# Kernel optimization log

Hardware: AMD Instinct MI355X
Metric: run time of the kernel (lower is better)

## Reference

```python
import jax, jax.numpy as jnp
import numpy as np

H = 16  # n_heads (from init_kwargs)


def l2norm(x, eps=1e-6):
    return x * jax.lax.rsqrt(jnp.sum(x * x, axis=-1, keepdims=True) + eps)


def causal_conv1d(x, w, b):
    # depthwise causal conv: x (B,T,D), w (D,k), b (D,). Matches torch
    # Conv1d(d,d,k,groups=d,padding=k-1) followed by [:, :, :T] truncation.
    T = x.shape[1]
    k = w.shape[1]
    xp = jnp.pad(x, ((0, 0), (k - 1, 0), (0, 0)))
    y = b
    for j in range(k):  # k=4 taps, fixed small loop
        y = y + xp[:, j:j + T, :] * w[:, j]
    return y


def setup_inputs():
    key = jax.random.key(0)
    ks = jax.random.split(key, 16)
    B, T, D, kc = 2, 2048, 1024, 4
    d = D // H
    s = 1.0 / np.sqrt(D)
    return {
        "x": jax.random.normal(ks[0], (B, T, D), jnp.float32),
        "Wq": jax.random.normal(ks[1], (D, D), jnp.float32) * s,
        "Wk": jax.random.normal(ks[2], (D, D), jnp.float32) * s,
        "Wv": jax.random.normal(ks[3], (D, D), jnp.float32) * s,
        "Wo": jax.random.normal(ks[4], (D, D), jnp.float32) * s,
        "Wg": jax.random.normal(ks[5], (D, D), jnp.float32) * s,
        "Wb": jax.random.normal(ks[6], (D, H), jnp.float32) * s,
        "cq_w": jax.random.normal(ks[7], (D, kc), jnp.float32) * 0.3,
        "cq_b": jax.random.normal(ks[8], (D,), jnp.float32) * 0.1,
        "ck_w": jax.random.normal(ks[9], (D, kc), jnp.float32) * 0.3,
        "ck_b": jax.random.normal(ks[10], (D,), jnp.float32) * 0.1,
        "cv_w": jax.random.normal(ks[11], (D, kc), jnp.float32) * 0.3,
        "cv_b": jax.random.normal(ks[12], (D,), jnp.float32) * 0.1,
        "nw": jnp.ones((d,), jnp.float32),
    }


def reference(x, Wq, Wk, Wv, Wo, Wg, Wb, cq_w, cq_b, ck_w, ck_b, cv_w, cv_b, nw):
    B, T, D = x.shape
    d = D // H
    q = l2norm(jax.nn.silu(causal_conv1d(x @ Wq, cq_w, cq_b)).reshape(B, T, H, d))
    q = q / jnp.sqrt(jnp.asarray(d, x.dtype))
    k = l2norm(jax.nn.silu(causal_conv1d(x @ Wk, ck_w, ck_b)).reshape(B, T, H, d))
    v = jax.nn.silu(causal_conv1d(x @ Wv, cv_w, cv_b)).reshape(B, T, H, d)
    gate = (x @ Wg).reshape(B, T, H, d)
    beta = jax.nn.sigmoid(x @ Wb)[..., None]  # (B,T,H,1)

    def step(S, qkvb):
        q_t, k_t, v_t, b_t = qkvb  # (B,H,d), (B,H,d), (B,H,d), (B,H,1)
        err = (v_t - jnp.einsum('bhk,bhkv->bhv', k_t, S)) * b_t
        S = S + jnp.einsum('bhk,bhv->bhkv', k_t, err)
        o_t = jnp.einsum('bhk,bhkv->bhv', q_t, S)
        return S, o_t

    S0 = jnp.zeros((B, H, d, d), x.dtype)
    xs = (q.transpose(1, 0, 2, 3), k.transpose(1, 0, 2, 3),
          v.transpose(1, 0, 2, 3), beta.transpose(1, 0, 2, 3))
    _, oT = jax.lax.scan(step, S0, xs)
    o = oT.transpose(1, 0, 2, 3)  # (B,T,H,d)
    # RMSNorm over head_dim
    o = o * jax.lax.rsqrt(jnp.mean(o * o, axis=-1, keepdims=True) + 1e-5) * nw
    o = o * jax.nn.silu(gate)
    return o.reshape(B, T, D) @ Wo
```

## Files before the change

kernel.cpp:

```cpp
#include <hip/hip_runtime.h>
#include <hip/hip_bf16.h>

typedef __attribute__((ext_vector_type(8))) short short8;
typedef __attribute__((ext_vector_type(4))) float f32x4;

#define TSEQ 2048
#define DMODEL 1024
#define NH 16
#define HD 64
#define PLANE 4194304

__device__ __forceinline__ ushort f2bf(float f) {
    union { float f; unsigned int u; } c; c.f = f;
    unsigned int u = c.u + 0x7fffu + ((c.u >> 16) & 1u);
    return (ushort)(u >> 16);
}

__device__ __forceinline__ float bf2f(ushort u) {
    union { unsigned int i; float f; } c; c.i = ((unsigned int)u) << 16;
    return c.f;
}

__device__ __forceinline__ void split2(float x, ushort& h, ushort& l) {
    h = f2bf(x);
    float r = x - bf2f(h);
    l = f2bf(r);
}

__device__ __forceinline__ float silu_f(float y) {
    return y / (1.f + __expf(-y));
}

__device__ __forceinline__ void gl_lds16(const float* g, float* l) {
    __builtin_amdgcn_global_load_lds(
        (__attribute__((address_space(1))) void*)g,
        (__attribute__((address_space(3))) void*)l, 16, 0, 0);
}

__global__ void gdn_cvt_x(const float* __restrict__ x, ushort* __restrict__ xb) {
    int i = blockIdx.x * 256 + threadIdx.x;
    float4 v = ((const float4*)x)[i];
    ushort4 o;
    o.x = f2bf(v.x); o.y = f2bf(v.y); o.z = f2bf(v.z); o.w = f2bf(v.w);
    ((ushort4*)xb)[i] = o;
}

__global__ void gdn_cvt_w(const float* __restrict__ Wq, const float* __restrict__ Wk,
                          const float* __restrict__ Wv, const float* __restrict__ Wg,
                          const float* __restrict__ Wo, ushort* __restrict__ wt) {
    __shared__ float tile[32][33];
    int z = blockIdx.z;
    const float* W = (z == 0) ? Wq : (z == 1) ? Wk : (z == 2) ? Wv : (z == 3) ? Wg : Wo;
    int n0 = blockIdx.x * 32, k0 = blockIdx.y * 32;
    int tx = threadIdx.x, ty = threadIdx.y;
    #pragma unroll
    for (int j = 0; j < 32; j += 8)
        tile[ty + j][tx] = W[(size_t)(k0 + ty + j) * DMODEL + n0 + tx];
    __syncthreads();
    ushort* o = wt + (size_t)z * DMODEL * DMODEL;
    #pragma unroll
    for (int j = 0; j < 32; j += 8)
        o[(size_t)(n0 + ty + j) * DMODEL + k0 + tx] = f2bf(tile[tx][ty + j]);
}

__global__ void gdn_beta(const float* __restrict__ x, const float* __restrict__ Wb,
                         float* __restrict__ betaT) {
    __shared__ float xs[16][DMODEL];
    int tid = threadIdx.x;
    int m0 = blockIdx.x * 16;
    #pragma unroll
    for (int i = 0; i < 16; i++) {
        int idx = i * 256 + tid;
        int row = idx >> 8, c4 = idx & 255;
        *(float4*)&xs[row][c4 * 4] =
            *(const float4*)&x[(size_t)(m0 + row) * DMODEL + c4 * 4];
    }
    __syncthreads();
    int h = tid & 15, mi = tid >> 4;
    float acc = 0.f;
    for (int k = 0; k < DMODEL; ++k)
        acc += xs[mi][k] * Wb[k * NH + h];
    int m = m0 + mi;
    int b = m >> 11, t = m & (TSEQ - 1);
    betaT[((b * NH + h) << 11) + t] = 1.f / (1.f + __expf(-acc));
}

#define LDT 40
__global__ __launch_bounds__(256) void gdn_gemm(const ushort* __restrict__ A,
                                                const ushort* __restrict__ Bt,
                                                float* __restrict__ outF,
                                                size_t planeStride) {
    __shared__ ushort As[128 * LDT];
    __shared__ ushort Bs[128 * LDT];
    int tid = threadIdx.x;
    int lane = tid & 63, wid = tid >> 6;
    int wm = wid & 1, wn = wid >> 1;
    int l15 = lane & 15, quad = lane >> 4;
    int bm = blockIdx.x, bn = blockIdx.y;
    const int K = DMODEL;

    f32x4 acc[4][4];
    #pragma unroll
    for (int i = 0; i < 4; i++)
        #pragma unroll
        for (int j = 0; j < 4; j++)
            acc[i][j] = (f32x4){0.f, 0.f, 0.f, 0.f};

    for (int kt = 0; kt < K; kt += 32) {
        __syncthreads();
        #pragma unroll
        for (int i = 0; i < 2; i++) {
            int ch = tid * 2 + i;
            int row = ch >> 2, q = ch & 3;
            uint4 av = ((const uint4*)A)[((bm * 128 + row) * K + kt) / 8 + q];
            *(uint4*)&As[row * LDT + q * 8] = av;
            uint4 bv = ((const uint4*)Bt)[((bn * 128 + row) * K + kt) / 8 + q];
            *(uint4*)&Bs[row * LDT + q * 8] = bv;
        }
        __syncthreads();
        short8 af[4], bf[4];
        #pragma unroll
        for (int i = 0; i < 4; i++) {
            af[i] = *(const short8*)&As[(wm * 64 + i * 16 + l15) * LDT + quad * 8];
            bf[i] = *(const short8*)&Bs[(wn * 64 + i * 16 + l15) * LDT + quad * 8];
        }
        #pragma unroll
        for (int mt = 0; mt < 4; mt++)
            #pragma unroll
            for (int nt = 0; nt < 4; nt++)
                acc[mt][nt] = __builtin_amdgcn_mfma_f32_16x16x32_bf16(
                    af[mt], bf[nt], acc[mt][nt], 0, 0, 0);
    }

    #pragma unroll
    for (int mt = 0; mt < 4; mt++)
        #pragma unroll
        for (int nt = 0; nt < 4; nt++)
            #pragma unroll
            for (int r = 0; r < 4; r++) {
                int row = bm * 128 + wm * 64 + mt * 16 + quad * 4 + r;
                int col = bn * 128 + wn * 64 + nt * 16 + l15;
                outF[(size_t)(col >> 10) * planeStride + (size_t)row * 1024 + (col & 1023)]
                    = acc[mt][nt][r];
            }
}

__global__ void gdn_conv(const float* __restrict__ pre,
                         const float* __restrict__ cqw, const float* __restrict__ cqb,
                         const float* __restrict__ ckw, const float* __restrict__ ckb,
                         const float* __restrict__ cvw, const float* __restrict__ cvb,
                         float* __restrict__ qn, float* __restrict__ kn, float* __restrict__ vn) {
    int m = blockIdx.x;
    int which = blockIdx.y;
    int t = m & (TSEQ - 1);
    const float* cw = (which == 0) ? cqw : (which == 1) ? ckw : cvw;
    const float* cb = (which == 0) ? cqb : (which == 1) ? ckb : cvb;
    float* dst = (which == 0) ? qn : (which == 1) ? kn : vn;
    int c = threadIdx.x * 4;

    float w[4][4];
    #pragma unroll
    for (int i = 0; i < 4; i++) {
        float4 t4 = ((const float4*)cw)[c + i];
        w[i][0] = t4.x; w[i][1] = t4.y; w[i][2] = t4.z; w[i][3] = t4.w;
    }
    float4 bias = ((const float4*)cb)[threadIdx.x];
    float y[4] = {bias.x, bias.y, bias.z, bias.w};

    const float* src = pre + (size_t)which * PLANE + (size_t)m * DMODEL + c;
    #pragma unroll
    for (int j = 0; j < 4; j++) {
        int tt = t - 3 + j;
        if (tt >= 0) {
            float4 xv = *(const float4*)(src + (long)(j - 3) * DMODEL);
            y[0] += xv.x * w[0][j];
            y[1] += xv.y * w[1][j];
            y[2] += xv.z * w[2][j];
            y[3] += xv.w * w[3][j];
        }
    }
    #pragma unroll
    for (int i = 0; i < 4; i++) y[i] = silu_f(y[i]);

    if (which < 2) {
        float ss = y[0]*y[0] + y[1]*y[1] + y[2]*y[2] + y[3]*y[3];
        ss += __shfl_xor(ss, 1);
        ss += __shfl_xor(ss, 2);
        ss += __shfl_xor(ss, 4);
        ss += __shfl_xor(ss, 8);
        float sc = rsqrtf(ss + 1e-6f);
        if (which == 0) sc *= 0.125f;
        #pragma unroll
        for (int i = 0; i < 4; i++) y[i] *= sc;
    }
    float4 o; o.x = y[0]; o.y = y[1]; o.z = y[2]; o.w = y[3];
    ((float4*)(dst + (size_t)m * 1024))[threadIdx.x] = o;
}

__global__ __launch_bounds__(256) void gdn_chunk(
    const float* __restrict__ kn, const float* __restrict__ vn,
    const float* __restrict__ betaT,
    ushort* __restrict__ WTst, ushort* __restrict__ U0st,
    float* __restrict__ Pst, float* __restrict__ Rst)
{
    __shared__ ushort Khi[64 * 72], Klo[64 * 72];
    __shared__ ushort KThi[64 * 72], KTlo[64 * 72];
    __shared__ ushort XThi[128 * 72], XTlo[128 * 72];
    __shared__ ushort Mneghi[64 * 72], Mneglo[64 * 72];
    __shared__ float  Xf[64 * 132];
    __shared__ float  MmDiag[4 * 16 * 20];
    __shared__ float  bet[64];

    int c = blockIdx.x, bh = blockIdx.y;
    int b = bh >> 4, h = bh & 15;
    int tid = threadIdx.x;
    int w = tid >> 6, lane = tid & 63;
    int l15 = lane & 15, quad = lane >> 4;
    size_t gbase = ((size_t)(b * TSEQ + c * 64)) * DMODEL + h * 64;
    size_t u = (size_t)bh * 32 + c;

    if (tid < 64) bet[tid] = betaT[((size_t)bh << 11) + c * 64 + tid];
    #pragma unroll
    for (int i = 0; i < 18; i++) {
        ((uint*)XThi)[tid + 256 * i] = 0u;
        ((uint*)XTlo)[tid + 256 * i] = 0u;
    }
    __syncthreads();

    #pragma unroll
    for (int i = 0; i < 4; i++) {
        int idx = tid + 256 * i;
        int r = idx >> 4, c4 = (idx & 15) * 4;
        float4 kv = *(const float4*)&kn[gbase + (size_t)r * DMODEL + c4];
        float4 vv = *(const float4*)&vn[gbase + (size_t)r * DMODEL + c4];
        float br = bet[r];
        float4 xk; xk.x = br * kv.x; xk.y = br * kv.y; xk.z = br * kv.z; xk.w = br * kv.w;
        float4 xv; xv.x = br * vv.x; xv.y = br * vv.y; xv.z = br * vv.z; xv.w = br * vv.w;
        *(float4*)&Xf[r * 132 + c4] = xk;
        *(float4*)&Xf[r * 132 + 64 + c4] = xv;
        ushort h0, l0, h1, l1, h2, l2, h3, l3;
        split2(kv.x, h0, l0); split2(kv.y, h1, l1);
        split2(kv.z, h2, l2); split2(kv.w, h3, l3);
        ((uint*)&Khi[r * 72 + c4])[0] = (uint)h0 | ((uint)h1 << 16);
        ((uint*)&Khi[r * 72 + c4])[1] = (uint)h2 | ((uint)h3 << 16);
        ((uint*)&Klo[r * 72 + c4])[0] = (uint)l0 | ((uint)l1 << 16);
        ((uint*)&Klo[r * 72 + c4])[1] = (uint)l2 | ((uint)l3 << 16);
        KThi[(c4 + 0) * 72 + r] = h0; KThi[(c4 + 1) * 72 + r] = h1;
        KThi[(c4 + 2) * 72 + r] = h2; KThi[(c4 + 3) * 72 + r] = h3;
        KTlo[(c4 + 0) * 72 + r] = l0; KTlo[(c4 + 1) * 72 + r] = l1;
        KTlo[(c4 + 2) * 72 + r] = l2; KTlo[(c4 + 3) * 72 + r] = l3;
    }
    __syncthreads();

    {
        f32x4 mAcc[4];
        #pragma unroll
        for (int tn = 0; tn < 4; tn++) mAcc[tn] = (f32x4){0.f, 0.f, 0.f, 0.f};
        #pragma unroll
        for (int ks = 0; ks < 2; ks++) {
            short8 aH = *(const short8*)&Khi[(16 * w + l15) * 72 + ks * 32 + quad * 8];
            short8 aL = *(const short8*)&Klo[(16 * w + l15) * 72 + ks * 32 + quad * 8];
            #pragma unroll
            for (int tn = 0; tn < 4; tn++) {
                short8 bH = *(const short8*)&Khi[(16 * tn + l15) * 72 + ks * 32 + quad * 8];
                short8 bL = *(const short8*)&Klo[(16 * tn + l15) * 72 + ks * 32 + quad * 8];
                mAcc[tn] = __builtin_amdgcn_mfma_f32_16x16x32_bf16(aH, bH, mAcc[tn], 0, 0, 0);
                mAcc[tn] = __builtin_amdgcn_mfma_f32_16x16x32_bf16(aH, bL, mAcc[tn], 0, 0, 0);
                mAcc[tn] = __builtin_amdgcn_mfma_f32_16x16x32_bf16(aL, bH, mAcc[tn], 0, 0, 0);
            }
        }
        #pragma unroll
        for (int tn = 0; tn < 4; tn++) {
            #pragma unroll
            for (int r = 0; r < 4; r++) {
                int row = 16 * w + quad * 4 + r;
                int col = tn * 16 + l15;
                float val = mAcc[tn][r] * bet[row];
                ushort hh = 0, ll = 0;
                if (col < row) {
                    float nv = -val;
                    hh = f2bf(nv);
                    ll = f2bf(nv - bf2f(hh));
                }
                Mneghi[row * 72 + col] = hh;
                Mneglo[row * 72 + col] = ll;
                if (tn == w) MmDiag[w * 320 + (row & 15) * 20 + l15] = val;
            }
        }
    }
    __syncthreads();

    #pragma unroll 1
    for (int st = 0; st < 4; st++) {
        int tb = st * 16;
        if (st) {
            f32x4 acc2[2];
            #pragma unroll
            for (int e = 0; e < 2; e++) {
                int tn = 2 * w + e;
                #pragma unroll
                for (int r = 0; r < 4; r++)
                    acc2[e][r] = Xf[(tb + quad * 4 + r) * 132 + tn * 16 + l15];
            }
            #pragma unroll
            for (int ks = 0; ks < 2; ks++) {
                short8 aH = *(const short8*)&Mneghi[(tb + l15) * 72 + ks * 32 + quad * 8];
                short8 aL = *(const short8*)&Mneglo[(tb + l15) * 72 + ks * 32 + quad * 8];
                #pragma unroll
                for (int e = 0; e < 2; e++) {
                    int tn = 2 * w + e;
                    short8 bH = *(const short8*)&XThi[(tn * 16 + l15) * 72 + ks * 32 + quad * 8];
                    short8 bL = *(const short8*)&XTlo[(tn * 16 + l15) * 72 + ks * 32 + quad * 8];
                    acc2[e] = __builtin_amdgcn_mfma_f32_16x16x32_bf16(aH, bH, acc2[e], 0, 0, 0);
                    acc2[e] = __builtin_amdgcn_mfma_f32_16x16x32_bf16(aH, bL, acc2[e], 0, 0, 0);
                    acc2[e] = __builtin_amdgcn_mfma_f32_16x16x32_bf16(aL, bH, acc2[e], 0, 0, 0);
                }
            }
            #pragma unroll
            for (int e = 0; e < 2; e++) {
                int tn = 2 * w + e;
                #pragma unroll
                for (int r = 0; r < 4; r++)
                    Xf[(tb + quad * 4 + r) * 132 + tn * 16 + l15] = acc2[e][r];
            }
        }
        __syncthreads();

        if (tid < 128) {
            const int j = tid;
            const float* MD = &MmDiag[st * 320];
            float xr[16];
            #pragma unroll
            for (int sb = 0; sb < 4; sb++) {
                float b4[4];
                #pragma unroll
                for (int i = 0; i < 4; i++)
                    b4[i] = Xf[(tb + sb * 4 + i) * 132 + j];
                #pragma unroll
                for (int u4 = 0; u4 < sb; u4++) {
                    #pragma unroll
                    for (int i = 0; i < 4; i++) {
                        float4 m4 = *(const float4*)&MD[(sb * 4 + i) * 20 + u4 * 4];
                        b4[i] -= m4.x * xr[u4 * 4 + 0] + m4.y * xr[u4 * 4 + 1]
                               + m4.z * xr[u4 * 4 + 2] + m4.w * xr[u4 * 4 + 3];
                    }
                }
                float x0 = b4[0];
                float x1 = b4[1] - MD[(sb * 4 + 1) * 20 + sb * 4 + 0] * x0;
                float x2 = b4[2] - MD[(sb * 4 + 2) * 20 + sb * 4 + 0] * x0
                                 - MD[(sb * 4 + 2) * 20 + sb * 4 + 1] * x1;
                float x3 = b4[3] - MD[(sb * 4 + 3) * 20 + sb * 4 + 0] * x0
                                 - MD[(sb * 4 + 3) * 20 + sb * 4 + 1] * x1
                                 - MD[(sb * 4 + 3) * 20 + sb * 4 + 2] * x2;
                xr[sb * 4 + 0] = x0; xr[sb * 4 + 1] = x1;
                xr[sb * 4 + 2] = x2; xr[sb * 4 + 3] = x3;
            }
            ushort hs[16], ls[16];
            #pragma unroll
            for (int i = 0; i < 16; i++) split2(xr[i], hs[i], ls[i]);
            uint4 ph0, ph1, pl0, pl1;
            ph0.x = (uint)hs[0] | ((uint)hs[1] << 16);  ph0.y = (uint)hs[2] | ((uint)hs[3] << 16);
            ph0.z = (uint)hs[4] | ((uint)hs[5] << 16);  ph0.w = (uint)hs[6] | ((uint)hs[7] << 16);
            ph1.x = (uint)hs[8] | ((uint)hs[9] << 16);  ph1.y = (uint)hs[10] | ((uint)hs[11] << 16);
            ph1.z = (uint)hs[12] | ((uint)hs[13] << 16); ph1.w = (uint)hs[14] | ((uint)hs[15] << 16);
            pl0.x = (uint)ls[0] | ((uint)ls[1] << 16);  pl0.y = (uint)ls[2] | ((uint)ls[3] << 16);
            pl0.z = (uint)ls[4] | ((uint)ls[5] << 16);  pl0.w = (uint)ls[6] | ((uint)ls[7] << 16);
            pl1.x = (uint)ls[8] | ((uint)ls[9] << 16);  pl1.y = (uint)ls[10] | ((uint)ls[11] << 16);
            pl1.z = (uint)ls[12] | ((uint)ls[13] << 16); pl1.w = (uint)ls[14] | ((uint)ls[15] << 16);
            *(uint4*)&XThi[j * 72 + tb] = ph0;  *(uint4*)&XThi[j * 72 + tb + 8] = ph1;
            *(uint4*)&XTlo[j * 72 + tb] = pl0;  *(uint4*)&XTlo[j * 72 + tb + 8] = pl1;
            if (j < 64) {
                ushort* wdst = WTst + u * 4096 + j * 64 + tb;
                *(uint4*)wdst = ph0; *(uint4*)(wdst + 8) = ph1;
            } else {
                ushort* udst = U0st + u * 4096 + (size_t)tb * 64 + (j - 64);
                #pragma unroll
                for (int i = 0; i < 16; i++) udst[i * 64] = hs[i];
            }
        }
        __syncthreads();
    }

    {
        f32x4 pAcc[4], rAcc[4];
        #pragma unroll
        for (int tn = 0; tn < 4; tn++) {
            pAcc[tn] = (f32x4){0.f, 0.f, 0.f, 0.f};
            rAcc[tn] = (f32x4){0.f, 0.f, 0.f, 0.f};
        }
        #pragma unroll
        for (int ks = 0; ks < 2; ks++) {
            short8 aH = *(const short8*)&XThi[(16 * w + l15) * 72 + ks * 32 + quad * 8];
            short8 aL = *(const short8*)&XTlo[(16 * w + l15) * 72 + ks * 32 + quad * 8];
            short8 cH = *(const short8*)&KThi[(16 * w + l15) * 72 + ks * 32 + quad * 8];
            short8 cL = *(const short8*)&KTlo[(16 * w + l15) * 72 + ks * 32 + quad * 8];
            #pragma unroll
            for (int tn = 0; tn < 4; tn++) {
                short8 bH = *(const short8*)&KThi[(16 * tn + l15) * 72 + ks * 32 + quad * 8];
                short8 bL = *(const short8*)&KTlo[(16 * tn + l15) * 72 + ks * 32 + quad * 8];
                pAcc[tn] = __builtin_amdgcn_mfma_f32_16x16x32_bf16(aH, bH, pAcc[tn], 0, 0, 0);
                pAcc[tn] = __builtin_amdgcn_mfma_f32_16x16x32_bf16(aH, bL, pAcc[tn], 0, 0, 0);
                pAcc[tn] = __builtin_amdgcn_mfma_f32_16x16x32_bf16(aL, bH, pAcc[tn], 0, 0, 0);
                short8 uH = *(const short8*)&XThi[(64 + 16 * tn + l15) * 72 + ks * 32 + quad * 8];
                short8 uL = *(const short8*)&XTlo[(64 + 16 * tn + l15) * 72 + ks * 32 + quad * 8];
                rAcc[tn] = __builtin_amdgcn_mfma_f32_16x16x32_bf16(cH, uH, rAcc[tn], 0, 0, 0);
                rAcc[tn] = __builtin_amdgcn_mfma_f32_16x16x32_bf16(cH, uL, rAcc[tn], 0, 0, 0);
                rAcc[tn] = __builtin_amdgcn_mfma_f32_16x16x32_bf16(cL, uH, rAcc[tn], 0, 0, 0);
            }
        }
        float* Po = Pst + u * 4096;
        float* Ro = Rst + u * 4096;
        #pragma unroll
        for (int tn = 0; tn < 4; tn++) {
            #pragma unroll
            for (int r = 0; r < 4; r++) {
                int row = 16 * w + quad * 4 + r;
                int col = tn * 16 + l15;
                Po[row * 64 + col] = pAcc[tn][r];
                Ro[row * 64 + col] = rAcc[tn][r];
            }
        }
    }
}

__global__ __launch_bounds__(256) void gdn_sstep(const float* __restrict__ Pst,
                                                 const float* __restrict__ Rst,
                                                 float* __restrict__ S0st)
{
    __shared__ float PTl[2][4096];
    __shared__ float Ssh[64][17];
    int bh = blockIdx.x >> 2, cg = blockIdx.x & 3;
    int tid = threadIdx.x;
    int t0 = (tid & 15) * 4;
    int j = tid >> 4;
    int jg = cg * 16 + j;
    int wv = tid >> 6, ln = tid & 63;

    #pragma unroll
    for (int i = 0; i < 4; i++) Ssh[t0 + i][j] = 0.f;

    {
        size_t ub0 = (size_t)bh * 32 * 4096;
        #pragma unroll
        for (int q = 0; q < 4; q++) {
            int seg = q * 4 + wv;
            gl_lds16(Pst + ub0 + seg * 256 + ln * 4, &PTl[0][seg * 256]);
        }
    }
    __syncthreads();

    for (int c = 0; c < 32; c++) {
        size_t ub = ((size_t)bh * 32 + c) * 4096;
        int cur = c & 1;
        if (c + 1 < 32) {
            size_t ub2 = ub + 4096;
            #pragma unroll
            for (int q = 0; q < 4; q++) {
                int seg = q * 4 + wv;
                gl_lds16(Pst + ub2 + seg * 256 + ln * 4, &PTl[cur ^ 1][seg * 256]);
            }
        }
        float sold[4], acc[4];
        #pragma unroll
        for (int i = 0; i < 4; i++) {
            sold[i] = Ssh[t0 + i][j];
            acc[i] = Rst[ub + (size_t)(t0 + i) * 64 + jg] + sold[i];
        }
        float sub0 = 0.f, sub1 = 0.f, sub2 = 0.f, sub3 = 0.f;
        #pragma unroll 8
        for (int uu = 0; uu < 64; uu++) {
            float4 pt = *(const float4*)&PTl[cur][uu * 64 + t0];
            float sv = Ssh[uu][j];
            sub0 = fmaf(pt.x, sv, sub0);
            sub1 = fmaf(pt.y, sv, sub1);
            sub2 = fmaf(pt.z, sv, sub2);
            sub3 = fmaf(pt.w, sv, sub3);
        }
        __syncthreads();
        Ssh[t0 + 0][j] = acc[0] - sub0;
        Ssh[t0 + 1][j] = acc[1] - sub1;
        Ssh[t0 + 2][j] = acc[2] - sub2;
        Ssh[t0 + 3][j] = acc[3] - sub3;
        #pragma unroll
        for (int i = 0; i < 4; i++)
            S0st[ub + (size_t)(t0 + i) * 64 + jg] = sold[i];
        __syncthreads();
    }
}

__global__ __launch_bounds__(256) void gdn_opass(
    const float* __restrict__ qn, const float* __restrict__ kn,
    const float* __restrict__ S0st, const ushort* __restrict__ WTst,
    const ushort* __restrict__ U0st, float* __restrict__ otmp2)
{
    __shared__ float Qs[64][65];
    __shared__ float KE[64][65];
    __shared__ float S0s[64][65];
    __shared__ float GT[4096];
    __shared__ ushort Wu[4096];
    __shared__ ushort Uu[4096];

    int c = blockIdx.x, bh = blockIdx.y;
    int b = bh >> 4, h = bh & 15;
    int tid = threadIdx.x;
    size_t gbase = ((size_t)(b * TSEQ + c * 64)) * DMODEL + h * 64;
    size_t u = (size_t)bh * 32 + c;

    #pragma unroll
    for (int i = 0; i < 4; i++) {
        int idx = tid + 256 * i;
        int r = idx >> 4, d4 = (idx & 15) * 4;
        float4 qv = *(const float4*)&qn[gbase + (size_t)r * DMODEL + d4];
        float4 kv = *(const float4*)&kn[gbase + (size_t)r * DMODEL + d4];
        float4 sv = *(const float4*)&S0st[u * 4096 + (size_t)idx * 4];
        Qs[r][d4 + 0] = qv.x; Qs[r][d4 + 1] = qv.y; Qs[r][d4 + 2] = qv.z; Qs[r][d4 + 3] = qv.w;
        KE[r][d4 + 0] = kv.x; KE[r][d4 + 1] = kv.y; KE[r][d4 + 2] = kv.z; KE[r][d4 + 3] = kv.w;
        S0s[r][d4 + 0] = sv.x; S0s[r][d4 + 1] = sv.y; S0s[r][d4 + 2] = sv.z; S0s[r][d4 + 3] = sv.w;
    }
    #pragma unroll
    for (int i = 0; i < 2; i++) {
        int idx = tid + 256 * i;
        uint4 w8 = *(const uint4*)&WTst[u * 4096 + (size_t)idx * 8];
        uint4 u8 = *(const uint4*)&U0st[u * 4096 + (size_t)idx * 8];
        *(uint4*)&Wu[idx * 8] = w8;
        *(uint4*)&Uu[idx * 8] = u8;
    }
    __syncthreads();

    int t0 = (tid & 15) * 4, s0 = (tid >> 4) * 4;

    float g[4][4];
    #pragma unroll
    for (int i = 0; i < 4; i++)
        #pragma unroll
        for (int j = 0; j < 4; j++) g[i][j] = 0.f;
    #pragma unroll 8
    for (int kk = 0; kk < 64; kk++) {
        float qt[4], kt[4];
        #pragma unroll
        for (int i = 0; i < 4; i++) qt[i] = Qs[t0 + i][kk];
        #pragma unroll
        for (int j = 0; j < 4; j++) kt[j] = KE[s0 + j][kk];
        #pragma unroll
        for (int i = 0; i < 4; i++)
            #pragma unroll
            for (int j = 0; j < 4; j++) g[i][j] = fmaf(qt[i], kt[j], g[i][j]);
    }
    float e[4][4];
    #pragma unroll
    for (int i = 0; i < 4; i++)
        #pragma unroll
        for (int j = 0; j < 4; j++) e[i][j] = 0.f;
    #pragma unroll 8
    for (int uu = 0; uu < 64; uu++) {
        ushort4 wv = *(const ushort4*)&Wu[uu * 64 + t0];
        float w0 = bf2f(wv.x), w1 = bf2f(wv.y), w2 = bf2f(wv.z), w3 = bf2f(wv.w);
        float s4[4];
        #pragma unroll
        for (int j = 0; j < 4; j++) s4[j] = S0s[uu][s0 + j];
        #pragma unroll
        for (int j = 0; j < 4; j++) {
            e[0][j] = fmaf(w0, s4[j], e[0][j]);
            e[1][j] = fmaf(w1, s4[j], e[1][j]);
            e[2][j] = fmaf(w2, s4[j], e[2][j]);
            e[3][j] = fmaf(w3, s4[j], e[3][j]);
        }
    }
    #pragma unroll
    for (int i = 0; i < 4; i++)
        #pragma unroll
        for (int jj = 0; jj < 4; jj++)
            GT[(s0 + jj) * 64 + t0 + i] = (s0 + jj <= t0 + i) ? g[i][jj] : 0.f;
    __syncthreads();
    #pragma unroll
    for (int i = 0; i < 4; i++) {
        ushort4 uv = *(const ushort4*)&Uu[(t0 + i) * 64 + s0];
        KE[t0 + i][s0 + 0] = bf2f(uv.x) - e[i][0];
        KE[t0 + i][s0 + 1] = bf2f(uv.y) - e[i][1];
        KE[t0 + i][s0 + 2] = bf2f(uv.z) - e[i][2];
        KE[t0 + i][s0 + 3] = bf2f(uv.w) - e[i][3];
    }
    __syncthreads();

    float o[4][4];
    #pragma unroll
    for (int i = 0; i < 4; i++)
        #pragma unroll
        for (int j = 0; j < 4; j++) o[i][j] = 0.f;
    #pragma unroll 8
    for (int kk = 0; kk < 64; kk++) {
        float qt[4], s4[4];
        #pragma unroll
        for (int i = 0; i < 4; i++) qt[i] = Qs[t0 + i][kk];
        #pragma unroll
        for (int j = 0; j < 4; j++) s4[j] = S0s[kk][s0 + j];
        #pragma unroll
        for (int i = 0; i < 4; i++)
            #pragma unroll
            for (int j = 0; j < 4; j++) o[i][j] = fmaf(qt[i], s4[j], o[i][j]);
    }
    #pragma unroll 8
    for (int ss = 0; ss < 64; ss++) {
        float4 gt = *(const float4*)&GT[ss * 64 + t0];
        float e4[4];
        #pragma unroll
        for (int j = 0; j < 4; j++) e4[j] = KE[ss][s0 + j];
        #pragma unroll
        for (int j = 0; j < 4; j++) {
            o[0][j] = fmaf(gt.x, e4[j], o[0][j]);
            o[1][j] = fmaf(gt.y, e4[j], o[1][j]);
            o[2][j] = fmaf(gt.z, e4[j], o[2][j]);
            o[3][j] = fmaf(gt.w, e4[j], o[3][j]);
        }
    }
    size_t obase = ((size_t)bh * 16 + (s0 >> 2)) * TSEQ + c * 64;
    #pragma unroll
    for (int i = 0; i < 4; i++) {
        float4 ov; ov.x = o[i][0]; ov.y = o[i][1]; ov.z = o[i][2]; ov.w = o[i][3];
        ((float4*)otmp2)[obase + t0 + i] = ov;
    }
}

__global__ void gdn_fuse(const float* __restrict__ otmp2, const float* __restrict__ pre,
                         const float* __restrict__ nw, ushort* __restrict__ ofused) {
    int m = blockIdx.x;
    int b = m >> 11, t = m & (TSEQ - 1);
    int tid = threadIdx.x;
    float4 o = ((const float4*)otmp2)[((size_t)((b * NH + (tid >> 4)) * 16 + (tid & 15))) * TSEQ + t];
    float ss = o.x*o.x + o.y*o.y + o.z*o.z + o.w*o.w;
    ss += __shfl_xor(ss, 1);
    ss += __shfl_xor(ss, 2);
    ss += __shfl_xor(ss, 4);
    ss += __shfl_xor(ss, 8);
    float r = rsqrtf(ss * (1.f / 64.f) + 1e-5f);
    float4 nwv = ((const float4*)nw)[tid & 15];
    float4 g = ((const float4*)(pre + 3 * (size_t)PLANE + (size_t)m * DMODEL))[tid];
    ushort4 out;
    out.x = f2bf(o.x * r * nwv.x * silu_f(g.x));
    out.y = f2bf(o.y * r * nwv.y * silu_f(g.y));
    out.z = f2bf(o.z * r * nwv.z * silu_f(g.z));
    out.w = f2bf(o.w * r * nwv.w * silu_f(g.w));
    ((ushort4*)ofused)[m * 256 + tid] = out;
}

extern "C" void kernel_launch(void* const* d_in, const int* in_sizes, int n_in,
                              void* d_out, int out_size, void* d_ws, size_t ws_size,
                              hipStream_t stream) {
    const float* x    = (const float*)d_in[0];
    const float* Wq   = (const float*)d_in[1];
    const float* Wk   = (const float*)d_in[2];
    const float* Wv   = (const float*)d_in[3];
    const float* Wo   = (const float*)d_in[4];
    const float* Wg   = (const float*)d_in[5];
    const float* Wb   = (const float*)d_in[6];
    const float* cq_w = (const float*)d_in[7];
    const float* cq_b = (const float*)d_in[8];
    const float* ck_w = (const float*)d_in[9];
    const float* ck_b = (const float*)d_in[10];
    const float* cv_w = (const float*)d_in[11];
    const float* cv_b = (const float*)d_in[12];
    const float* nw   = (const float*)d_in[13];

    char* ws = (char*)d_ws;
    ushort* xb     = (ushort*)(ws);
    ushort* wt     = (ushort*)(ws + 8388608);
    float*  pre    = (float*)(ws + 18874368);
    float*  qn     = (float*)(ws + 85983232);
    float*  kn     = (float*)(ws + 102760448);
    float*  vn     = (float*)(ws + 119537664);
    float*  betaT  = (float*)(ws + 136314880);
    float*  otmp2  = (float*)(ws + 136577024);
    ushort* ofused = (ushort*)(ws + 153354240);

    float*  Pst  = pre;
    float*  Rst  = pre + PLANE;
    float*  S0st = pre + 2 * PLANE;
    ushort* WTst = xb;
    ushort* U0st = ofused;

    gdn_cvt_x<<<4096, 256, 0, stream>>>(x, xb);
    gdn_cvt_w<<<dim3(32, 32, 5), dim3(32, 8), 0, stream>>>(Wq, Wk, Wv, Wg, Wo, wt);
    gdn_beta<<<256, 256, 0, stream>>>(x, Wb, betaT);
    gdn_gemm<<<dim3(32, 32), 256, 0, stream>>>(xb, wt, pre, (size_t)PLANE);
    gdn_conv<<<dim3(4096, 3), 256, 0, stream>>>(pre, cq_w, cq_b, ck_w, ck_b, cv_w, cv_b,
                                                qn, kn, vn);
    gdn_chunk<<<dim3(32, 32), 256, 0, stream>>>(kn, vn, betaT, WTst, U0st, Pst, Rst);
    gdn_sstep<<<128, 256, 0, stream>>>(Pst, Rst, S0st);
    gdn_opass<<<dim3(32, 32), 256, 0, stream>>>(qn, kn, S0st, WTst, U0st, otmp2);
    gdn_fuse<<<4096, 256, 0, stream>>>(otmp2, pre, nw, ofused);
    gdn_gemm<<<dim3(32, 8), 256, 0, stream>>>(ofused, wt + 4 * 1024 * 1024,
                                              (float*)d_out, (size_t)0);
}
```

Measured before the change: 459.5 us.

## Triple-buffer P/R chunk loads and transpose S in gdn_sstep to use one barrier

The state-propagation kernel now prefetches both P and the R chunk (stored transposed by the producer) two chunks ahead into triple-buffered LDS. It keeps the running state transposed and double-buffered so each step needs a single barrier and reads S as float4. Manual vmcnt waits replace __syncthreads. This targets the serial latency of the 32-chunk recurrence, at the cost of fragile hand-tuned waitcnt counts and more LDS use.

After: 433.6 us. 5.6% less time.

```diff
diff --git a/kernel.cpp b/kernel.cpp
--- a/kernel.cpp
+++ b/kernel.cpp
@@ -417,7 +417,7 @@
                 int row = 16 * w + quad * 4 + r;
                 int col = tn * 16 + l15;
                 Po[row * 64 + col] = pAcc[tn][r];
-                Ro[row * 64 + col] = rAcc[tn][r];
+                Ro[col * 64 + row] = rAcc[tn][r];
             }
         }
     }
@@ -427,64 +427,78 @@
                                                  const float* __restrict__ Rst,
                                                  float* __restrict__ S0st)
 {
-    __shared__ float PTl[2][4096];
-    __shared__ float Ssh[64][17];
+    __shared__ float PTl[3][4096];
+    __shared__ float Rl[3][1024];
+    __shared__ float SshT[2][16][72];
+
     int bh = blockIdx.x >> 2, cg = blockIdx.x & 3;
     int tid = threadIdx.x;
     int t0 = (tid & 15) * 4;
-    int j = tid >> 4;
+    int j  = tid >> 4;
     int jg = cg * 16 + j;
     int wv = tid >> 6, ln = tid & 63;
 
-    #pragma unroll
-    for (int i = 0; i < 4; i++) Ssh[t0 + i][j] = 0.f;
-
-    {
-        size_t ub0 = (size_t)bh * 32 * 4096;
-        #pragma unroll
-        for (int q = 0; q < 4; q++) {
-            int seg = q * 4 + wv;
-            gl_lds16(Pst + ub0 + seg * 256 + ln * 4, &PTl[0][seg * 256]);
-        }
-    }
-    __syncthreads();
-
-    for (int c = 0; c < 32; c++) {
-        size_t ub = ((size_t)bh * 32 + c) * 4096;
-        int cur = c & 1;
-        if (c + 1 < 32) {
-            size_t ub2 = ub + 4096;
-            #pragma unroll
-            for (int q = 0; q < 4; q++) {
-                int seg = q * 4 + wv;
-                gl_lds16(Pst + ub2 + seg * 256 + ln * 4, &PTl[cur ^ 1][seg * 256]);
-            }
-        }
-        float sold[4], acc[4];
-        #pragma unroll
-        for (int i = 0; i < 4; i++) {
-            sold[i] = Ssh[t0 + i][j];
-            acc[i] = Rst[ub + (size_t)(t0 + i) * 64 + jg] + sold[i];
-        }
+    size_t ubase = (size_t)bh * 32 * 4096;
+
+    *(float4*)&SshT[0][j][t0] = (float4){0.f, 0.f, 0.f, 0.f};
+
+    #pragma unroll
+    for (int t = 0; t < 2; t++) {
+        size_t ub = ubase + (size_t)t * 4096;
+        #pragma unroll
+        for (int q = 0; q < 4; q++)
+            gl_lds16(Pst + ub + (wv * 4 + q) * 256 + ln * 4, &PTl[t][(wv * 4 + q) * 256]);
+        gl_lds16(Rst + ub + cg * 1024 + wv * 256 + ln * 4, &Rl[t][wv * 256]);
+    }
+    asm volatile("s_waitcnt vmcnt(5)" ::: "memory");
+    asm volatile("s_waitcnt lgkmcnt(0)" ::: "memory");
+    __builtin_amdgcn_s_barrier();
+
+    int cur3 = 0;
+    #pragma unroll 1
+    for (int c = 0; c < 32; ++c) {
+        int cur = c & 1, nxt = cur ^ 1;
+        if (c + 2 < 32) {
+            int b3 = cur3 + 2; if (b3 >= 3) b3 -= 3;
+            size_t ub2 = ubase + (size_t)(c + 2) * 4096;
+            #pragma unroll
+            for (int q = 0; q < 4; q++)
+                gl_lds16(Pst + ub2 + (wv * 4 + q) * 256 + ln * 4, &PTl[b3][(wv * 4 + q) * 256]);
+            gl_lds16(Rst + ub2 + cg * 1024 + wv * 256 + ln * 4, &Rl[b3][wv * 256]);
+        }
+        float4 sold = *(const float4*)&SshT[cur][j][t0];
+        size_t ub = ubase + (size_t)c * 4096;
+        S0st[ub + (size_t)(t0 + 0) * 64 + jg] = sold.x;
+        S0st[ub + (size_t)(t0 + 1) * 64 + jg] = sold.y;
+        S0st[ub + (size_t)(t0 + 2) * 64 + jg] = sold.z;
+        S0st[ub + (size_t)(t0 + 3) * 64 + jg] = sold.w;
+        float4 racc = *(const float4*)&Rl[cur3][j * 64 + t0];
         float sub0 = 0.f, sub1 = 0.f, sub2 = 0.f, sub3 = 0.f;
-        #pragma unroll 8
-        for (int uu = 0; uu < 64; uu++) {
-            float4 pt = *(const float4*)&PTl[cur][uu * 64 + t0];
-            float sv = Ssh[uu][j];
-            sub0 = fmaf(pt.x, sv, sub0);
-            sub1 = fmaf(pt.y, sv, sub1);
-            sub2 = fmaf(pt.z, sv, sub2);
-            sub3 = fmaf(pt.w, sv, sub3);
-        }
-        __syncthreads();
-        Ssh[t0 + 0][j] = acc[0] - sub0;
-        Ssh[t0 + 1][j] = acc[1] - sub1;
-        Ssh[t0 + 2][j] = acc[2] - sub2;
-        Ssh[t0 + 3][j] = acc[3] - sub3;
-        #pragma unroll
-        for (int i = 0; i < 4; i++)
-            S0st[ub + (size_t)(t0 + i) * 64 + jg] = sold[i];
-        __syncthreads();
+        #pragma unroll
+        for (int u4 = 0; u4 < 16; u4++) {
+            float4 sv = *(const float4*)&SshT[cur][j][u4 * 4];
+            #pragma unroll
+            for (int e = 0; e < 4; e++) {
+                float4 pt = *(const float4*)&PTl[cur3][(u4 * 4 + e) * 64 + t0];
+                float s1 = (e == 0) ? sv.x : (e == 1) ? sv.y : (e == 2) ? sv.z : sv.w;
+                sub0 = fmaf(pt.x, s1, sub0);
+                sub1 = fmaf(pt.y, s1, sub1);
+                sub2 = fmaf(pt.z, s1, sub2);
+                sub3 = fmaf(pt.w, s1, sub3);
+            }
+        }
+        float4 snew;
+        snew.x = sold.x + racc.x - sub0;
+        snew.y = sold.y + racc.y - sub1;
+        snew.z = sold.z + racc.z - sub2;
+        snew.w = sold.w + racc.w - sub3;
+        *(float4*)&SshT[nxt][j][t0] = snew;
+        if (c == 0)       { asm volatile("s_waitcnt vmcnt(9)"  ::: "memory"); }
+        else if (c < 30)  { asm volatile("s_waitcnt vmcnt(13)" ::: "memory"); }
+        else if (c == 30) { asm volatile("s_waitcnt vmcnt(8)"  ::: "memory"); }
+        asm volatile("s_waitcnt lgkmcnt(0)" ::: "memory");
+        __builtin_amdgcn_s_barrier();
+        cur3 += 1; if (cur3 >= 3) cur3 -= 3;
     }
 }
 
```
